# Kernel optimization log

Hardware: AMD Instinct MI355X
Metric: run time of the kernel (lower is better)

Reference implementation:

```python
import jax, jax.numpy as jnp
import numpy as np

B, M, S, N, DIN, C = 2048, 5, 128, 128, 64, 32
MID = C // 2  # 16
EPS = 1e-5
NEG_SLOPE = 0.2


def setup_inputs() -> dict:
    key = jax.random.key(0)
    ks = jax.random.split(key, 13)
    sc = lambda fan: 1.0 / np.sqrt(fan)
    return {
        "x_global": jax.random.normal(ks[0], (B, N, C), jnp.float32),
        "x_local": jax.random.normal(ks[1], (B * M, S, DIN), jnp.float32),
        "W_lin": jax.random.normal(ks[2], (C, DIN), jnp.float32) * sc(DIN),
        "b_lin": jnp.zeros((C,), jnp.float32),
        "W_att": jax.random.normal(ks[3], (C,), jnp.float32) * sc(C),  # Conv2d(C,1,1) weight
        "Wa": jax.random.normal(ks[4], (MID, C), jnp.float32) * sc(C),
        "Wb": jax.random.normal(ks[5], (MID, C), jnp.float32) * sc(C),
        "Wc": jax.random.normal(ks[6], (MID, C), jnp.float32) * sc(C),
        "Wn": jax.random.normal(ks[7], (MID, MID), jnp.float32) * sc(MID),
        "Wl": jax.random.normal(ks[8], (MID, MID), jnp.float32) * sc(MID),
        "Wd": jax.random.normal(ks[9], (C, 2 * MID), jnp.float32) * sc(2 * MID),
        "bn_gamma": jnp.ones((C,), jnp.float32),
        "bn_beta": jnp.zeros((C,), jnp.float32),
    }


def reference(x_global, x_local, W_lin, b_lin, W_att, Wa, Wb, Wc, Wn, Wl, Wd, bn_gamma, bn_beta):
    # --- Motion_Aggregation_Module.forward ---
    xl = x_local.reshape(B, M, S, DIN)
    xl = jnp.einsum('bmsd,cd->bmsc', xl, W_lin) + b_lin          # Linear(64,32)
    curves = jnp.transpose(xl, (0, 3, 1, 2))                      # [B,C,M,S]
    x = jnp.transpose(x_global, (0, 2, 1))                        # [B,C,N]

    # --- Correlation_Module.forward ---
    att = jnp.einsum('c,bcms->bms', W_att, curves)                # line_conv_att -> [B,M,S]
    inter = jnp.einsum('bcms,bms->bcm', curves, jax.nn.softmax(att, axis=-1))  # [B,C,M]
    intra = jnp.einsum('bcms,bms->bcs', curves, jax.nn.softmax(att, axis=-2))  # [B,C,S]

    inter = jnp.einsum('oc,bcm->bom', Wa, inter)                  # conva -> [B,MID,M]
    intra = jnp.einsum('oc,bcs->bos', Wb, intra)                  # convb -> [B,MID,S]
    x_logits = jnp.einsum('oc,bcn->bno', Wc, x)                   # convc^T -> [B,N,MID]

    a_inter = jax.nn.softmax(jnp.einsum('bno,bom->bnm', x_logits, inter), axis=-1)  # [B,N,M]
    a_intra = jax.nn.softmax(jnp.einsum('bno,bos->bns', x_logits, intra), axis=-1)  # [B,N,S]

    v_inter = jnp.einsum('po,bom->bmp', Wn, inter)                # convn^T -> [B,M,MID]
    v_intra = jnp.einsum('po,bos->bsp', Wl, intra)                # convl^T -> [B,S,MID]

    f_inter = jnp.einsum('bnm,bmp->bnp', a_inter, v_inter)        # [B,N,MID]
    f_intra = jnp.einsum('bns,bsp->bnp', a_intra, v_intra)        # [B,N,MID]
    feat = jnp.concatenate([f_inter, f_intra], axis=-1)           # [B,N,2*MID]
    feat = jnp.einsum('oc,bnc->bon', Wd, feat)                    # convd conv -> [B,C,N]

    # BatchNorm1d (training mode: batch stats over (B, N), biased variance)
    mean = feat.mean(axis=(0, 2), keepdims=True)
    var = feat.var(axis=(0, 2), keepdims=True)
    feat = (feat - mean) * jax.lax.rsqrt(var + EPS)
    feat = feat * bn_gamma[None, :, None] + bn_beta[None, :, None]

    out = x + feat                                                # residual
    out = jnp.where(out >= 0, out, NEG_SLOPE * out)               # leaky_relu(0.2)
    return jnp.transpose(out, (0, 2, 1))                          # [B,N,C]
```

## Files before the change

kernel.cpp:

```cpp
#include <hip/hip_runtime.h>
#include <math.h>

#define NB 2048
typedef float f32x4 __attribute__((ext_vector_type(4)));
typedef float f32x2 __attribute__((ext_vector_type(2)));

#define P_WAL 0
#define P_WBL 1024
#define P_WLBL 2048
#define P_WNAL 3072
#define P_WEFF 4096
#define P_BWA 4160
#define P_BWB 4176
#define P_BWL 4192
#define P_BWN 4208
#define P_C0  4224

#define WS_BNPART 4352
#define WS_COEF   135424
#define WS_SMALL  135488
#define WS_BIG_I  463168
#define WS_BIG_V  (463168 + 4194304)
#define WS_FEAT16 (463168 + 8388608)

__device__ __forceinline__ unsigned short f2bf(float f) {
  unsigned int u = __float_as_uint(f);
  u += 0x7fffu + ((u >> 16) & 1u);
  return (unsigned short)(u >> 16);
}
__device__ __forceinline__ unsigned int pack2bf(float lo, float hi) {
  return (unsigned int)f2bf(lo) | ((unsigned int)f2bf(hi) << 16);
}
__device__ __forceinline__ float bflo(unsigned int u) { return __uint_as_float(u << 16); }
__device__ __forceinline__ float bfhi(unsigned int u) { return __uint_as_float(u & 0xffff0000u); }

#define BSTAGE(MASK, HALF)                                        \
  { const bool hi_ = (lane & (MASK)) != 0;                        \
    _Pragma("unroll")                                             \
    for (int k_ = 0; k_ < (HALF); ++k_) {                         \
      float mine_ = hi_ ? a[k_ + (HALF)] : a[k_];                 \
      float oth_  = hi_ ? a[k_] : a[k_ + (HALF)];                 \
      a[k_] = mine_ + __shfl_xor(oth_, (MASK));                   \
    } }

__global__ __launch_bounds__(256) void k0_pre(const float* __restrict__ W_lin,
                                              const float* __restrict__ b_lin,
                                              const float* __restrict__ W_att,
                                              const float* __restrict__ Wa,
                                              const float* __restrict__ Wb,
                                              const float* __restrict__ Wn,
                                              const float* __restrict__ Wl,
                                              float* __restrict__ pre) {
  int t = threadIdx.x;
  for (int i = t; i < 1024; i += 256) {
    int o = i >> 6, d = i & 63;
    float sa = 0.f, sb = 0.f;
    for (int c = 0; c < 32; ++c) {
      float wl = W_lin[c * 64 + d];
      sa += Wa[o * 32 + c] * wl;
      sb += Wb[o * 32 + c] * wl;
    }
    pre[P_WAL + i] = sa;
    pre[P_WBL + i] = sb;
  }
  if (t < 64) {
    float s = 0.f;
    for (int c = 0; c < 32; ++c) s += W_att[c] * W_lin[c * 64 + t];
    pre[P_WEFF + t] = s;
  }
  if (t < 16) {
    float sa = 0.f, sb = 0.f;
    for (int c = 0; c < 32; ++c) {
      sa += Wa[t * 32 + c] * b_lin[c];
      sb += Wb[t * 32 + c] * b_lin[c];
    }
    pre[P_BWA + t] = sa;
    pre[P_BWB + t] = sb;
  }
  if (t == 0) {
    float s = 0.f;
    for (int c = 0; c < 32; ++c) s += W_att[c] * b_lin[c];
    pre[P_C0] = s;
  }
  __syncthreads();
  for (int i = t; i < 1024; i += 256) {
    int p_ = i >> 6, d = i & 63;
    float sl = 0.f, sn = 0.f;
    for (int o = 0; o < 16; ++o) {
      sl += Wl[p_ * 16 + o] * pre[P_WBL + o * 64 + d];
      sn += Wn[p_ * 16 + o] * pre[P_WAL + o * 64 + d];
    }
    pre[P_WLBL + i] = sl;
    pre[P_WNAL + i] = sn;
  }
  if (t < 16) {
    float sl = 0.f, sn = 0.f;
    for (int o = 0; o < 16; ++o) {
      sl += Wl[t * 16 + o] * pre[P_BWB + o];
      sn += Wn[t * 16 + o] * pre[P_BWA + o];
    }
    pre[P_BWL + t] = sl;
    pre[P_BWN + t] = sn;
  }
}

__global__ __launch_bounds__(1024, 2) void k1a(
    const float* __restrict__ xl_all, const float* __restrict__ pre,
    float* __restrict__ p_small, float* __restrict__ bigI,
    float* __restrict__ bigV) {
  __shared__ __align__(16) float xaggi[128 * 68];
  __shared__ f32x4 scratch5[5][16][16];
  __shared__ float pe[5][16];
  __shared__ float xagg_inter[5][64];

  const int t = threadIdx.x;
  const int b = blockIdx.x;
  const int lane = t & 63;
  const int w = t >> 6;
  const int q = lane >> 4;
  const int i16 = lane & 15;

  const float* xl = xl_all + (size_t)b * (5 * 128 * 64);
  const f32x4 weff4 = ((const f32x4*)(pre + P_WEFF))[i16];
  const float c0 = pre[P_C0];

  const float* xb = xl + (size_t)(8 * w + q) * 64 + 4 * i16;

  f32x4 xA[2], xB[2], acc[2];
  float Zk[2];
  #pragma unroll
  for (int k = 0; k < 2; ++k) {
    acc[k] = (f32x4)0.f;
    Zk[k] = 0.f;
    xA[k] = *(const f32x4*)(xb + k * 256);
  }

  #pragma unroll
  for (int m = 0; m < 5; ++m) {
    f32x4* xc = (m & 1) ? xB : xA;
    f32x4* xn = (m & 1) ? xA : xB;
    if (m < 4) {
      const float* np = xb + (size_t)(m + 1) * 8192;
      #pragma unroll
      for (int k = 0; k < 2; ++k) xn[k] = *(const f32x4*)(np + k * 256);
    }
    float a0, a1;
    {
      f32x4 p0 = xc[0] * weff4, p1 = xc[1] * weff4;
      a0 = p0.x + p0.y + p0.z + p0.w;
      a1 = p1.x + p1.y + p1.z + p1.w;
    }
    #pragma unroll
    for (int mask = 1; mask <= 8; mask <<= 1) {
      a0 += __shfl_xor(a0, mask);
      a1 += __shfl_xor(a1, mask);
    }
    float e0 = __expf(a0 + c0), e1 = __expf(a1 + c0);
    Zk[0] += e0; Zk[1] += e1;
    f32x4 pim;
    {
      f32x4 pr0 = e0 * xc[0];
      f32x4 pr1 = e1 * xc[1];
      acc[0] += pr0; acc[1] += pr1;
      pim = pr0 + pr1;
    }
    float se = e0 + e1;
    #pragma unroll
    for (int mask = 16; mask <= 32; mask <<= 1) {
      pim.x += __shfl_xor(pim.x, mask);
      pim.y += __shfl_xor(pim.y, mask);
      pim.z += __shfl_xor(pim.z, mask);
      pim.w += __shfl_xor(pim.w, mask);
      se += __shfl_xor(se, mask);
    }
    if (lane < 16) {
      scratch5[m][w][i16] = pim;
      if (i16 == 0) pe[m][w] = se;
    }
  }

  #pragma unroll
  for (int k = 0; k < 2; ++k) {
    float invz = 1.f / Zk[k];
    f32x4 v = acc[k] * invz;
    int r = 8 * w + 4 * k + q;
    *(f32x4*)&xaggi[r * 68 + 4 * i16] = v;
  }
  __syncthreads();

  if (t < 320) {
    int mm = t >> 6, d = t & 63;
    const float* sp = (const float*)&scratch5[mm][0][0];
    float s = 0.f;
    #pragma unroll
    for (int j = 0; j < 16; ++j) s += sp[j * 64 + d];
    float sume = 0.f;
    #pragma unroll
    for (int j = 0; j < 16; ++j) sume += pe[mm][j];
    xagg_inter[mm][d] = s / sume;
  }
  __syncthreads();

  if (t < 512) {
    const int q2 = __builtin_amdgcn_readfirstlane(t >> 7);
    const int s2 = t & 127;
    const float* Wbase = pre + ((q2 < 2) ? P_WBL : P_WLBL) + (q2 & 1) * 512;
    const float* xrow = &xaggi[s2 * 68];
    float acc2[8];
    #pragma unroll
    for (int r = 0; r < 8; ++r) acc2[r] = 0.f;
    #pragma unroll
    for (int c = 0; c < 64; c += 4) {
      f32x4 xa = *(const f32x4*)(xrow + c);
      #pragma unroll
      for (int r = 0; r < 8; ++r)
        acc2[r] += xa.x * Wbase[r * 64 + c] + xa.y * Wbase[r * 64 + c + 1] +
                   xa.z * Wbase[r * 64 + c + 2] + xa.w * Wbase[r * 64 + c + 3];
    }
    const int bb = ((q2 < 2) ? P_BWB : P_BWL) + (q2 & 1) * 8;
    float* dst = ((q2 < 2) ? bigI : bigV) + (size_t)b * 2048 + s2 * 16 + (q2 & 1) * 8;
    f32x4 o0, o1;
    o0.x = acc2[0] + pre[bb + 0];
    o0.y = acc2[1] + pre[bb + 1];
    o0.z = acc2[2] + pre[bb + 2];
    o0.w = acc2[3] + pre[bb + 3];
    o1.x = acc2[4] + pre[bb + 4];
    o1.y = acc2[5] + pre[bb + 5];
    o1.z = acc2[6] + pre[bb + 6];
    o1.w = acc2[7] + pre[bb + 7];
    *(f32x4*)dst = o0;
    *(f32x4*)(dst + 4) = o1;
  } else if (t < 672) {
    int tt = t - 512;
    int o2 = tt & 31, mm = tt >> 5;
    const float* wr = pre + ((o2 < 16) ? (P_WAL + o2 * 64) : (P_WNAL + (o2 - 16) * 64));
    float p = 0.f;
    #pragma unroll
    for (int d = 0; d < 64; ++d) p += wr[d] * xagg_inter[mm][d];
    p += (o2 < 16) ? pre[P_BWA + o2] : pre[P_BWN + (o2 - 16)];
    float* os = p_small + (size_t)b * 160;
    if (o2 < 16) os[mm * 16 + o2] = p;
    else os[80 + mm * 16 + (o2 - 16)] = p;
  }
}

__global__ __launch_bounds__(128, 1) void k1b(
    const float* __restrict__ xg_all, const float* __restrict__ Wc_g,
    const float* __restrict__ Wd_g, const float* __restrict__ p_small,
    const float* __restrict__ bigI, const float* __restrict__ bigV,
    unsigned int* __restrict__ feat16, float* __restrict__ bn_part) {
  __shared__ f32x4 slabI[128][4];
  __shared__ f32x4 slabV[128][4];
  __shared__ float part1[2][32];
  __shared__ float part2[2][32];

  const int t = threadIdx.x;
  const int b = blockIdx.x;
  const int lane = t & 63;
  const int w = t >> 6;
  const int kmap = ((lane & 1) << 4) | ((lane & 2) << 2) | (lane & 4) |
                   ((lane >> 2) & 2) | ((lane >> 4) & 1);

  const f32x4* gI = (const f32x4*)(bigI + (size_t)b * 2048);
  const f32x4* gV = (const f32x4*)(bigV + (size_t)b * 2048);
  #pragma unroll
  for (int j = 0; j < 4; ++j) {
    ((f32x4*)slabI)[t + 128 * j] = gI[t + 128 * j];
    ((f32x4*)slabV)[t + 128 * j] = gV[t + 128 * j];
  }

  const f32x4* xgr = (const f32x4*)(xg_all + ((size_t)b * 128 + t) * 32);
  f32x4 xv[8];
  #pragma unroll
  for (int j = 0; j < 8; ++j) xv[j] = xgr[j];
  f32x4 xl4[4];
  #pragma unroll
  for (int o4 = 0; o4 < 4; ++o4) {
    f32x4 r;
    #pragma unroll
    for (int jj = 0; jj < 4; ++jj) {
      const int o = o4 * 4 + jj;
      f32x4 s = (f32x4)0.f;
      #pragma unroll
      for (int j = 0; j < 8; ++j) s += xv[j] * *(const f32x4*)(Wc_g + o * 32 + 4 * j);
      r[jj] = s.x + s.y + s.z + s.w;
    }
    xl4[o4] = r;
  }
  __syncthreads();

  float sum = 0.f;
  f32x4 fa[4];
  #pragma unroll
  for (int j = 0; j < 4; ++j) fa[j] = (f32x4)0.f;
  for (int i = 0; i < 128; ++i) {
    f32x4 d4 = xl4[0] * slabI[i][0] + xl4[1] * slabI[i][1] +
               xl4[2] * slabI[i][2] + xl4[3] * slabI[i][3];
    float e = __expf(d4.x + d4.y + d4.z + d4.w);
    sum += e;
    #pragma unroll
    for (int j = 0; j < 4; ++j) fa[j] += e * slabV[i][j];
  }
  const float inv = 1.f / sum;
  f32x4 fin[4];
  #pragma unroll
  for (int j = 0; j < 4; ++j) fin[j] = fa[j] * inv;

  const float* sm = p_small + (size_t)b * 160;
  float L[5], mx3 = -1e30f;
  #pragma unroll
  for (int mm = 0; mm < 5; ++mm) {
    float p = 0.f;
    #pragma unroll
    for (int o4 = 0; o4 < 4; ++o4) {
      #pragma unroll
      for (int jj = 0; jj < 4; ++jj) p += xl4[o4][jj] * sm[mm * 16 + o4 * 4 + jj];
    }
    L[mm] = p;
    mx3 = fmaxf(mx3, p);
  }
  float sum3 = 0.f;
  #pragma unroll
  for (int mm = 0; mm < 5; ++mm) { L[mm] = __expf(L[mm] - mx3); sum3 += L[mm]; }
  const float inv3 = 1.f / sum3;
  f32x4 fi[4];
  #pragma unroll
  for (int o4 = 0; o4 < 4; ++o4) {
    f32x4 r;
    #pragma unroll
    for (int jj = 0; jj < 4; ++jj) {
      float p = 0.f;
      #pragma unroll
      for (int mm = 0; mm < 5; ++mm) p += L[mm] * sm[80 + mm * 16 + o4 * 4 + jj];
      r[jj] = p * inv3;
    }
    fi[o4] = r;
  }

  f32x4 feat[8];
  #pragma unroll
  for (int o4 = 0; o4 < 8; ++o4) {
    f32x4 r;
    #pragma unroll
    for (int jj = 0; jj < 4; ++jj) {
      const int o = o4 * 4 + jj;
      f32x4 s = (f32x4)0.f;
      #pragma unroll
      for (int j = 0; j < 4; ++j) {
        s += fi[j]  * *(const f32x4*)(Wd_g + o * 32 + 4 * j);
        s += fin[j] * *(const f32x4*)(Wd_g + o * 32 + 16 + 4 * j);
      }
      r[jj] = s.x + s.y + s.z + s.w;
    }
    feat[o4] = r;
  }
  {
    unsigned int* op = feat16 + ((size_t)b * 128 + t) * 16;
    uint4 u0, u1, u2, u3;
    u0.x = pack2bf(feat[0].x, feat[0].y); u0.y = pack2bf(feat[0].z, feat[0].w);
    u0.z = pack2bf(feat[1].x, feat[1].y); u0.w = pack2bf(feat[1].z, feat[1].w);
    u1.x = pack2bf(feat[2].x, feat[2].y); u1.y = pack2bf(feat[2].z, feat[2].w);
    u1.z = pack2bf(feat[3].x, feat[3].y); u1.w = pack2bf(feat[3].z, feat[3].w);
    u2.x = pack2bf(feat[4].x, feat[4].y); u2.y = pack2bf(feat[4].z, feat[4].w);
    u2.z = pack2bf(feat[5].x, feat[5].y); u2.w = pack2bf(feat[5].z, feat[5].w);
    u3.x = pack2bf(feat[6].x, feat[6].y); u3.y = pack2bf(feat[6].z, feat[6].w);
    u3.z = pack2bf(feat[7].x, feat[7].y); u3.w = pack2bf(feat[7].z, feat[7].w);
    ((uint4*)op)[0] = u0;
    ((uint4*)op)[1] = u1;
    ((uint4*)op)[2] = u2;
    ((uint4*)op)[3] = u3;
  }

  {
    float a[32];
    #pragma unroll
    for (int o = 0; o < 32; ++o) a[o] = feat[o >> 2][o & 3];
    BSTAGE(1, 16) BSTAGE(2, 8) BSTAGE(4, 4) BSTAGE(8, 2) BSTAGE(16, 1)
    a[0] += __shfl_xor(a[0], 32);
    if (lane < 32) part1[w][kmap] = a[0];
  }
  {
    float a[32];
    #pragma unroll
    for (int o = 0; o < 32; ++o) { float v = feat[o >> 2][o & 3]; a[o] = v * v; }
    BSTAGE(1, 16) BSTAGE(2, 8) BSTAGE(4, 4) BSTAGE(8, 2) BSTAGE(16, 1)
    a[0] += __shfl_xor(a[0], 32);
    if (lane < 32) part2[w][kmap] = a[0];
  }
  __syncthreads();
  if (t < 64) {
    int c = t & 31, h = t >> 5;
    float v = h ? (part2[0][c] + part2[1][c]) : (part1[0][c] + part1[1][c]);
    bn_part[(size_t)b * 64 + h * 32 + c] = v;
  }
}

__global__ __launch_bounds__(256, 1) void k2_stats(const float* __restrict__ bn_part,
                                                   const float* __restrict__ gamma,
                                                   const float* __restrict__ beta,
                                                   float* __restrict__ coef) {
  __shared__ float red[2][4];
  const int c = blockIdx.x;
  const int t = threadIdx.x;
  const int lane = t & 63, w = t >> 6;
  float s1 = 0.f, s2 = 0.f;
  for (int bb = t; bb < NB; bb += 256) {
    s1 += bn_part[(size_t)bb * 64 + c];
    s2 += bn_part[(size_t)bb * 64 + c + 32];
  }
  #pragma unroll
  for (int mask = 1; mask <= 32; mask <<= 1) {
    s1 += __shfl_xor(s1, mask);
    s2 += __shfl_xor(s2, mask);
  }
  if (lane == 0) { red[0][w] = s1; red[1][w] = s2; }
  __syncthreads();
  if (t == 0) {
    float S1 = red[0][0] + red[0][1] + red[0][2] + red[0][3];
    float S2 = red[1][0] + red[1][1] + red[1][2] + red[1][3];
    const float inv = 1.f / (float)(NB * 128);
    float mean = S1 * inv;
    float var = S2 * inv - mean * mean;
    float scl = gamma[c] * rsqrtf(var + 1e-5f);
    coef[c] = scl;
    coef[32 + c] = beta[c] - mean * scl;
  }
}

__global__ __launch_bounds__(256) void k3_final(const float* __restrict__ xg,
                                                const unsigned int* __restrict__ feat16,
                                                float* __restrict__ out,
                                                const float* __restrict__ coef) {
  __shared__ float s_c[64];
  if (threadIdx.x < 64) s_c[threadIdx.x] = coef[threadIdx.x];
  __syncthreads();
  size_t i4 = (size_t)blockIdx.x * 256 + threadIdx.x;
  uint2 fu = ((const uint2*)feat16)[i4];
  float4 x = ((const float4*)xg)[i4];
  int c = (int)((i4 * 4) & 31);
  float4 r;
  r.x = x.x + bflo(fu.x) * s_c[c + 0] + s_c[32 + c + 0];
  r.y = x.y + bfhi(fu.x) * s_c[c + 1] + s_c[32 + c + 1];
  r.z = x.z + bflo(fu.y) * s_c[c + 2] + s_c[32 + c + 2];
  r.w = x.w + bfhi(fu.y) * s_c[c + 3] + s_c[32 + c + 3];
  r.x = r.x >= 0.f ? r.x : 0.2f * r.x;
  r.y = r.y >= 0.f ? r.y : 0.2f * r.y;
  r.z = r.z >= 0.f ? r.z : 0.2f * r.z;
  r.w = r.w >= 0.f ? r.w : 0.2f * r.w;
  ((float4*)out)[i4] = r;
}

extern "C" void kernel_launch(void* const* d_in, const int* in_sizes, int n_in,
                              void* d_out, int out_size, void* d_ws, size_t ws_size,
                              hipStream_t stream) {
  const float* xg    = (const float*)d_in[0];
  const float* xl    = (const float*)d_in[1];
  const float* W_lin = (const float*)d_in[2];
  const float* b_lin = (const float*)d_in[3];
  const float* W_att = (const float*)d_in[4];
  const float* Wa    = (const float*)d_in[5];
  const float* Wb    = (const float*)d_in[6];
  const float* Wc    = (const float*)d_in[7];
  const float* Wn    = (const float*)d_in[8];
  const float* Wl    = (const float*)d_in[9];
  const float* Wd    = (const float*)d_in[10];
  const float* gamma = (const float*)d_in[11];
  const float* beta  = (const float*)d_in[12];
  float* out = (float*)d_out;
  float* ws = (float*)d_ws;
  float* pre = ws;
  float* bn_part = ws + WS_BNPART;
  float* coef = ws + WS_COEF;
  float* p_small = ws + WS_SMALL;
  float* bigI = ws + WS_BIG_I;
  float* bigV = ws + WS_BIG_V;
  unsigned int* feat16 = (unsigned int*)(ws + WS_FEAT16);

  hipLaunchKernelGGL(k0_pre, dim3(1), dim3(256), 0, stream,
                     W_lin, b_lin, W_att, Wa, Wb, Wn, Wl, pre);
  hipLaunchKernelGGL(k1a, dim3(NB), dim3(1024), 0, stream, xl, pre, p_small, bigI, bigV);
  hipLaunchKernelGGL(k1b, dim3(NB), dim3(128), 0, stream,
                     xg, Wc, Wd, p_small, bigI, bigV, feat16, bn_part);
  hipLaunchKernelGGL(k2_stats, dim3(32), dim3(256), 0, stream, bn_part, gamma, beta, coef);
  hipLaunchKernelGGL(k3_final, dim3(8192), dim3(256), 0, stream, xg, feat16, out, coef);
}
```

Before: 196.7 us.

## Merge k1a and k1b into one kernel keeping intermediates in shared memory

Fuses the per-batch aggregation kernel and the attention/projection kernel into a single 1024-thread kernel. The bigI/bigV/p_small intermediates stay in LDS and are no longer written to and re-read from global memory, which removes about 33 MB of traffic and one launch. The second stage is re-partitioned across 8 threads per row instead of 1, with shuffle reductions, and the Wc projection overlaps with the inter-aggregation phase. The cost is heavier LDS use per block, which may cut occupancy, plus extra shuffle work.

```diff
diff --git a/kernel.cpp b/kernel.cpp
--- a/kernel.cpp
+++ b/kernel.cpp
@@ -18,10 +18,7 @@
 
 #define WS_BNPART 4352
 #define WS_COEF   135424
-#define WS_SMALL  135488
-#define WS_BIG_I  463168
-#define WS_BIG_V  (463168 + 4194304)
-#define WS_FEAT16 (463168 + 8388608)
+#define WS_FEAT16 140000
 
 __device__ __forceinline__ unsigned short f2bf(float f) {
   unsigned int u = __float_as_uint(f);
@@ -104,14 +101,23 @@
   }
 }
 
-__global__ __launch_bounds__(1024, 2) void k1a(
-    const float* __restrict__ xl_all, const float* __restrict__ pre,
-    float* __restrict__ p_small, float* __restrict__ bigI,
-    float* __restrict__ bigV) {
+__global__ __launch_bounds__(1024, 2) void k1_merged(
+    const float* __restrict__ xl_all, const float* __restrict__ xg_all,
+    const float* __restrict__ pre, const float* __restrict__ Wc_g,
+    const float* __restrict__ Wd_g, unsigned int* __restrict__ feat16,
+    float* __restrict__ bn_part) {
   __shared__ __align__(16) float xaggi[128 * 68];
-  __shared__ f32x4 scratch5[5][16][16];
-  __shared__ float pe[5][16];
-  __shared__ float xagg_inter[5][64];
+  __shared__ __align__(16) float RU[5120];
+  __shared__ __align__(16) float xlogL[128 * 20];
+  __shared__ float s_Wd[32][33];
+  __shared__ float pe[80];
+  __shared__ float xagg_inter[320];
+  __shared__ float s_small[160];
+  __shared__ float part1[16][33];
+  __shared__ float part2[16][33];
+
+  float* slabI = RU;
+  float* slabV = RU + 2560;
 
   const int t = threadIdx.x;
   const int b = blockIdx.x;
@@ -119,13 +125,16 @@
   const int w = t >> 6;
   const int q = lane >> 4;
   const int i16 = lane & 15;
+  const int n2 = t >> 3;
+  const int q3 = t & 7;
 
   const float* xl = xl_all + (size_t)b * (5 * 128 * 64);
   const f32x4 weff4 = ((const f32x4*)(pre + P_WEFF))[i16];
   const float c0 = pre[P_C0];
 
+  if (t < 1024) { int i = t; if (i < 1024) s_Wd[i >> 5][i & 31] = Wd_g[i]; }
+
   const float* xb = xl + (size_t)(8 * w + q) * 64 + 4 * i16;
-
   f32x4 xA[2], xB[2], acc[2];
   float Zk[2];
   #pragma unroll
@@ -134,7 +143,6 @@
     Zk[k] = 0.f;
     xA[k] = *(const f32x4*)(xb + k * 256);
   }
-
   #pragma unroll
   for (int m = 0; m < 5; ++m) {
     f32x4* xc = (m & 1) ? xB : xA;
@@ -174,11 +182,10 @@
       se += __shfl_xor(se, mask);
     }
     if (lane < 16) {
-      scratch5[m][w][i16] = pim;
-      if (i16 == 0) pe[m][w] = se;
-    }
-  }
-
+      ((f32x4*)RU)[(m * 16 + w) * 16 + i16] = pim;
+      if (i16 == 0) pe[m * 16 + w] = se;
+    }
+  }
   #pragma unroll
   for (int k = 0; k < 2; ++k) {
     float invz = 1.f / Zk[k];
@@ -190,14 +197,27 @@
 
   if (t < 320) {
     int mm = t >> 6, d = t & 63;
-    const float* sp = (const float*)&scratch5[mm][0][0];
+    const float* sp = RU + mm * 1024;
     float s = 0.f;
     #pragma unroll
     for (int j = 0; j < 16; ++j) s += sp[j * 64 + d];
     float sume = 0.f;
     #pragma unroll
-    for (int j = 0; j < 16; ++j) sume += pe[mm][j];
-    xagg_inter[mm][d] = s / sume;
+    for (int j = 0; j < 16; ++j) sume += pe[mm * 16 + j];
+    xagg_inter[mm * 64 + d] = s / sume;
+  } else if (t >= 896) {
+    int n = t - 896;
+    const f32x4* xgr = (const f32x4*)(xg_all + ((size_t)b * 128 + n) * 32);
+    f32x4 xv[8];
+    #pragma unroll
+    for (int j = 0; j < 8; ++j) xv[j] = xgr[j];
+    #pragma unroll
+    for (int o = 0; o < 16; ++o) {
+      f32x4 s = (f32x4)0.f;
+      #pragma unroll
+      for (int j = 0; j < 8; ++j) s += xv[j] * *(const f32x4*)(Wc_g + o * 32 + 4 * j);
+      xlogL[n * 20 + o] = s.x + s.y + s.z + s.w;
+    }
   }
   __syncthreads();
 
@@ -218,7 +238,7 @@
                    xa.z * Wbase[r * 64 + c + 2] + xa.w * Wbase[r * 64 + c + 3];
     }
     const int bb = ((q2 < 2) ? P_BWB : P_BWL) + (q2 & 1) * 8;
-    float* dst = ((q2 < 2) ? bigI : bigV) + (size_t)b * 2048 + s2 * 16 + (q2 & 1) * 8;
+    float* dst = ((q2 < 2) ? slabI : slabV) + s2 * 20 + (q2 & 1) * 8;
     f32x4 o0, o1;
     o0.x = acc2[0] + pre[bb + 0];
     o0.y = acc2[1] + pre[bb + 1];
@@ -236,85 +256,55 @@
     const float* wr = pre + ((o2 < 16) ? (P_WAL + o2 * 64) : (P_WNAL + (o2 - 16) * 64));
     float p = 0.f;
     #pragma unroll
-    for (int d = 0; d < 64; ++d) p += wr[d] * xagg_inter[mm][d];
+    for (int d = 0; d < 64; ++d) p += wr[d] * xagg_inter[mm * 64 + d];
     p += (o2 < 16) ? pre[P_BWA + o2] : pre[P_BWN + (o2 - 16)];
-    float* os = p_small + (size_t)b * 160;
-    if (o2 < 16) os[mm * 16 + o2] = p;
-    else os[80 + mm * 16 + (o2 - 16)] = p;
-  }
-}
-
-__global__ __launch_bounds__(128, 1) void k1b(
-    const float* __restrict__ xg_all, const float* __restrict__ Wc_g,
-    const float* __restrict__ Wd_g, const float* __restrict__ p_small,
-    const float* __restrict__ bigI, const float* __restrict__ bigV,
-    unsigned int* __restrict__ feat16, float* __restrict__ bn_part) {
-  __shared__ f32x4 slabI[128][4];
-  __shared__ f32x4 slabV[128][4];
-  __shared__ float part1[2][32];
-  __shared__ float part2[2][32];
-
-  const int t = threadIdx.x;
-  const int b = blockIdx.x;
-  const int lane = t & 63;
-  const int w = t >> 6;
-  const int kmap = ((lane & 1) << 4) | ((lane & 2) << 2) | (lane & 4) |
-                   ((lane >> 2) & 2) | ((lane >> 4) & 1);
-
-  const f32x4* gI = (const f32x4*)(bigI + (size_t)b * 2048);
-  const f32x4* gV = (const f32x4*)(bigV + (size_t)b * 2048);
-  #pragma unroll
-  for (int j = 0; j < 4; ++j) {
-    ((f32x4*)slabI)[t + 128 * j] = gI[t + 128 * j];
-    ((f32x4*)slabV)[t + 128 * j] = gV[t + 128 * j];
-  }
-
-  const f32x4* xgr = (const f32x4*)(xg_all + ((size_t)b * 128 + t) * 32);
-  f32x4 xv[8];
-  #pragma unroll
-  for (int j = 0; j < 8; ++j) xv[j] = xgr[j];
-  f32x4 xl4[4];
-  #pragma unroll
-  for (int o4 = 0; o4 < 4; ++o4) {
-    f32x4 r;
-    #pragma unroll
-    for (int jj = 0; jj < 4; ++jj) {
-      const int o = o4 * 4 + jj;
-      f32x4 s = (f32x4)0.f;
-      #pragma unroll
-      for (int j = 0; j < 8; ++j) s += xv[j] * *(const f32x4*)(Wc_g + o * 32 + 4 * j);
-      r[jj] = s.x + s.y + s.z + s.w;
-    }
-    xl4[o4] = r;
-  }
-  __syncthreads();
-
+    if (o2 < 16) s_small[mm * 16 + o2] = p;
+    else s_small[80 + mm * 16 + (o2 - 16)] = p;
+  }
+  __syncthreads();
+
+  f32x4 xlg[4];
+  #pragma unroll
+  for (int c = 0; c < 4; ++c) xlg[c] = *(const f32x4*)&xlogL[n2 * 20 + 4 * c];
   float sum = 0.f;
-  f32x4 fa[4];
-  #pragma unroll
-  for (int j = 0; j < 4; ++j) fa[j] = (f32x4)0.f;
-  for (int i = 0; i < 128; ++i) {
-    f32x4 d4 = xl4[0] * slabI[i][0] + xl4[1] * slabI[i][1] +
-               xl4[2] * slabI[i][2] + xl4[3] * slabI[i][3];
+  f32x4 fav[4];
+  #pragma unroll
+  for (int c = 0; c < 4; ++c) fav[c] = (f32x4)0.f;
+  #pragma unroll 4
+  for (int k = 0; k < 16; ++k) {
+    const int i = q3 + 8 * k;
+    const f32x4* rI = (const f32x4*)&slabI[i * 20];
+    f32x4 d4 = xlg[0] * rI[0] + xlg[1] * rI[1] + xlg[2] * rI[2] + xlg[3] * rI[3];
     float e = __expf(d4.x + d4.y + d4.z + d4.w);
     sum += e;
-    #pragma unroll
-    for (int j = 0; j < 4; ++j) fa[j] += e * slabV[i][j];
+    const f32x4* rV = (const f32x4*)&slabV[i * 20];
+    #pragma unroll
+    for (int c = 0; c < 4; ++c) fav[c] += e * rV[c];
+  }
+  #pragma unroll
+  for (int mask = 1; mask <= 4; mask <<= 1) {
+    sum += __shfl_xor(sum, mask);
+    #pragma unroll
+    for (int c = 0; c < 4; ++c) {
+      fav[c].x += __shfl_xor(fav[c].x, mask);
+      fav[c].y += __shfl_xor(fav[c].y, mask);
+      fav[c].z += __shfl_xor(fav[c].z, mask);
+      fav[c].w += __shfl_xor(fav[c].w, mask);
+    }
   }
   const float inv = 1.f / sum;
   f32x4 fin[4];
   #pragma unroll
-  for (int j = 0; j < 4; ++j) fin[j] = fa[j] * inv;
-
-  const float* sm = p_small + (size_t)b * 160;
+  for (int c = 0; c < 4; ++c) fin[c] = fav[c] * inv;
+
   float L[5], mx3 = -1e30f;
   #pragma unroll
   for (int mm = 0; mm < 5; ++mm) {
     float p = 0.f;
     #pragma unroll
-    for (int o4 = 0; o4 < 4; ++o4) {
-      #pragma unroll
-      for (int jj = 0; jj < 4; ++jj) p += xl4[o4][jj] * sm[mm * 16 + o4 * 4 + jj];
+    for (int c = 0; c < 4; ++c) {
+      #pragma unroll
+      for (int jj = 0; jj < 4; ++jj) p += xlg[c][jj] * s_small[mm * 16 + 4 * c + jj];
     }
     L[mm] = p;
     mx3 = fmaxf(mx3, p);
@@ -325,72 +315,61 @@
   const float inv3 = 1.f / sum3;
   f32x4 fi[4];
   #pragma unroll
-  for (int o4 = 0; o4 < 4; ++o4) {
+  for (int c = 0; c < 4; ++c) {
     f32x4 r;
     #pragma unroll
     for (int jj = 0; jj < 4; ++jj) {
       float p = 0.f;
       #pragma unroll
-      for (int mm = 0; mm < 5; ++mm) p += L[mm] * sm[80 + mm * 16 + o4 * 4 + jj];
+      for (int mm = 0; mm < 5; ++mm) p += L[mm] * s_small[80 + mm * 16 + 4 * c + jj];
       r[jj] = p * inv3;
     }
-    fi[o4] = r;
-  }
-
-  f32x4 feat[8];
-  #pragma unroll
-  for (int o4 = 0; o4 < 8; ++o4) {
-    f32x4 r;
-    #pragma unroll
-    for (int jj = 0; jj < 4; ++jj) {
-      const int o = o4 * 4 + jj;
-      f32x4 s = (f32x4)0.f;
-      #pragma unroll
-      for (int j = 0; j < 4; ++j) {
-        s += fi[j]  * *(const f32x4*)(Wd_g + o * 32 + 4 * j);
-        s += fin[j] * *(const f32x4*)(Wd_g + o * 32 + 16 + 4 * j);
+    fi[c] = r;
+  }
+  float fo[4];
+  #pragma unroll
+  for (int j = 0; j < 4; ++j) {
+    const int o = 4 * q3 + j;
+    float p = 0.f;
+    #pragma unroll
+    for (int c = 0; c < 4; ++c) {
+      #pragma unroll
+      for (int jj = 0; jj < 4; ++jj) {
+        p += fi[c][jj] * s_Wd[o][4 * c + jj];
+        p += fin[c][jj] * s_Wd[o][16 + 4 * c + jj];
       }
-      r[jj] = s.x + s.y + s.z + s.w;
-    }
-    feat[o4] = r;
+    }
+    fo[j] = p;
   }
   {
-    unsigned int* op = feat16 + ((size_t)b * 128 + t) * 16;
-    uint4 u0, u1, u2, u3;
-    u0.x = pack2bf(feat[0].x, feat[0].y); u0.y = pack2bf(feat[0].z, feat[0].w);
-    u0.z = pack2bf(feat[1].x, feat[1].y); u0.w = pack2bf(feat[1].z, feat[1].w);
-    u1.x = pack2bf(feat[2].x, feat[2].y); u1.y = pack2bf(feat[2].z, feat[2].w);
-    u1.z = pack2bf(feat[3].x, feat[3].y); u1.w = pack2bf(feat[3].z, feat[3].w);
-    u2.x = pack2bf(feat[4].x, feat[4].y); u2.y = pack2bf(feat[4].z, feat[4].w);
-    u2.z = pack2bf(feat[5].x, feat[5].y); u2.w = pack2bf(feat[5].z, feat[5].w);
-    u3.x = pack2bf(feat[6].x, feat[6].y); u3.y = pack2bf(feat[6].z, feat[6].w);
-    u3.z = pack2bf(feat[7].x, feat[7].y); u3.w = pack2bf(feat[7].z, feat[7].w);
-    ((uint4*)op)[0] = u0;
-    ((uint4*)op)[1] = u1;
-    ((uint4*)op)[2] = u2;
-    ((uint4*)op)[3] = u3;
-  }
-
+    uint2 u;
+    u.x = pack2bf(fo[0], fo[1]);
+    u.y = pack2bf(fo[2], fo[3]);
+    ((uint2*)feat16)[(size_t)b * 1024 + n2 * 8 + q3] = u;
+  }
+  const int omap = 4 * q3 + 2 * ((lane >> 3) & 1) + ((lane >> 4) & 1);
   {
-    float a[32];
-    #pragma unroll
-    for (int o = 0; o < 32; ++o) a[o] = feat[o >> 2][o & 3];
-    BSTAGE(1, 16) BSTAGE(2, 8) BSTAGE(4, 4) BSTAGE(8, 2) BSTAGE(16, 1)
+    float a[4];
+    #pragma unroll
+    for (int j = 0; j < 4; ++j) a[j] = fo[j];
+    BSTAGE(8, 2) BSTAGE(16, 1)
     a[0] += __shfl_xor(a[0], 32);
-    if (lane < 32) part1[w][kmap] = a[0];
+    if (lane < 32) part1[w][omap] = a[0];
   }
   {
-    float a[32];
-    #pragma unroll
-    for (int o = 0; o < 32; ++o) { float v = feat[o >> 2][o & 3]; a[o] = v * v; }
-    BSTAGE(1, 16) BSTAGE(2, 8) BSTAGE(4, 4) BSTAGE(8, 2) BSTAGE(16, 1)
+    float a[4];
+    #pragma unroll
+    for (int j = 0; j < 4; ++j) a[j] = fo[j] * fo[j];
+    BSTAGE(8, 2) BSTAGE(16, 1)
     a[0] += __shfl_xor(a[0], 32);
-    if (lane < 32) part2[w][kmap] = a[0];
+    if (lane < 32) part2[w][omap] = a[0];
   }
   __syncthreads();
   if (t < 64) {
     int c = t & 31, h = t >> 5;
-    float v = h ? (part2[0][c] + part2[1][c]) : (part1[0][c] + part1[1][c]);
+    float v = 0.f;
+    #pragma unroll
+    for (int j = 0; j < 16; ++j) v += h ? part2[j][c] : part1[j][c];
     bn_part[(size_t)b * 64 + h * 32 + c] = v;
   }
 }
@@ -471,16 +450,12 @@
   float* pre = ws;
   float* bn_part = ws + WS_BNPART;
   float* coef = ws + WS_COEF;
-  float* p_small = ws + WS_SMALL;
-  float* bigI = ws + WS_BIG_I;
-  float* bigV = ws + WS_BIG_V;
   unsigned int* feat16 = (unsigned int*)(ws + WS_FEAT16);
 
   hipLaunchKernelGGL(k0_pre, dim3(1), dim3(256), 0, stream,
                      W_lin, b_lin, W_att, Wa, Wb, Wn, Wl, pre);
-  hipLaunchKernelGGL(k1a, dim3(NB), dim3(1024), 0, stream, xl, pre, p_small, bigI, bigV);
-  hipLaunchKernelGGL(k1b, dim3(NB), dim3(128), 0, stream,
-                     xg, Wc, Wd, p_small, bigI, bigV, feat16, bn_part);
+  hipLaunchKernelGGL(k1_merged, dim3(NB), dim3(1024), 0, stream,
+                     xl, xg, pre, Wc, Wd, feat16, bn_part);
   hipLaunchKernelGGL(k2_stats, dim3(32), dim3(256), 0, stream, bn_part, gamma, beta, coef);
   hipLaunchKernelGGL(k3_final, dim3(8192), dim3(256), 0, stream, xg, feat16, out, coef);
 }
```

Measured after the change: 246.1 us. 25.1% more time.

## Split k1b softmax-attention loop across four waves with LDS reduction

Applied to the files above, without the earlier changes.

k1b now launches 256 threads per batch instead of 128. Each wave handles a quarter of the 128 intra keys for two query rows, and the partial exp-sums and weighted value accumulators are reduced through padded shared memory. The xlogit projection and p_small values are staged in LDS, and the slabs are padded to a row stride of 20 to avoid bank conflicts. This is meant to shorten the serial 128-iteration loop per thread and raise occupancy, at the cost of extra barriers, a shared-memory reduction and more LDS use.

```diff
diff --git a/kernel.cpp b/kernel.cpp
--- a/kernel.cpp
+++ b/kernel.cpp
@@ -244,13 +244,16 @@
   }
 }
 
-__global__ __launch_bounds__(128, 1) void k1b(
+__global__ __launch_bounds__(256, 4) void k1b(
     const float* __restrict__ xg_all, const float* __restrict__ Wc_g,
     const float* __restrict__ Wd_g, const float* __restrict__ p_small,
     const float* __restrict__ bigI, const float* __restrict__ bigV,
     unsigned int* __restrict__ feat16, float* __restrict__ bn_part) {
-  __shared__ f32x4 slabI[128][4];
-  __shared__ f32x4 slabV[128][4];
+  __shared__ __align__(16) float UN[10240];
+  float* slabI = UN;
+  float* slabV = UN + 2560;
+  float* xlogL = UN + 5120;
+  __shared__ float s_sm[160];
   __shared__ float part1[2][32];
   __shared__ float part2[2][32];
 
@@ -258,134 +261,216 @@
   const int b = blockIdx.x;
   const int lane = t & 63;
   const int w = t >> 6;
-  const int kmap = ((lane & 1) << 4) | ((lane & 2) << 2) | (lane & 4) |
-                   ((lane >> 2) & 2) | ((lane >> 4) & 1);
-
-  const f32x4* gI = (const f32x4*)(bigI + (size_t)b * 2048);
-  const f32x4* gV = (const f32x4*)(bigV + (size_t)b * 2048);
+
+  {
+    const f32x4* gI = (const f32x4*)(bigI + (size_t)b * 2048);
+    const f32x4* gV = (const f32x4*)(bigV + (size_t)b * 2048);
+    #pragma unroll
+    for (int j = 0; j < 2; ++j) {
+      int idx = t + 256 * j;
+      int row = idx >> 2, c4 = idx & 3;
+      *(f32x4*)&slabI[row * 20 + 4 * c4] = gI[idx];
+      *(f32x4*)&slabV[row * 20 + 4 * c4] = gV[idx];
+    }
+  }
+  if (t < 128) {
+    const int n = t;
+    const f32x4* xgr = (const f32x4*)(xg_all + ((size_t)b * 128 + n) * 32);
+    f32x4 xv[8];
+    #pragma unroll
+    for (int j = 0; j < 8; ++j) xv[j] = xgr[j];
+    #pragma unroll
+    for (int o4 = 0; o4 < 4; ++o4) {
+      f32x4 r;
+      #pragma unroll
+      for (int jj = 0; jj < 4; ++jj) {
+        const int o = o4 * 4 + jj;
+        f32x4 s = (f32x4)0.f;
+        #pragma unroll
+        for (int j = 0; j < 8; ++j) s += xv[j] * *(const f32x4*)(Wc_g + o * 32 + 4 * j);
+        r[jj] = s.x + s.y + s.z + s.w;
+      }
+      *(f32x4*)&xlogL[n * 20 + 4 * o4] = r;
+    }
+  }
+  if (t >= 96) {
+    int i2 = t - 96;
+    s_sm[i2] = p_small[(size_t)b * 160 + i2];
+  }
+  __syncthreads();
+
+  const int n0 = lane, n1 = lane + 64;
+  f32x4 xlg0[4], xlg1[4];
   #pragma unroll
-  for (int j = 0; j < 4; ++j) {
-    ((f32x4*)slabI)[t + 128 * j] = gI[t + 128 * j];
-    ((f32x4*)slabV)[t + 128 * j] = gV[t + 128 * j];
-  }
-
-  const f32x4* xgr = (const f32x4*)(xg_all + ((size_t)b * 128 + t) * 32);
-  f32x4 xv[8];
+  for (int c = 0; c < 4; ++c) {
+    xlg0[c] = *(const f32x4*)&xlogL[n0 * 20 + 4 * c];
+    xlg1[c] = *(const f32x4*)&xlogL[n1 * 20 + 4 * c];
+  }
+
+  float s0 = 0.f, s1 = 0.f;
+  f32x4 fav0[4], fav1[4];
   #pragma unroll
-  for (int j = 0; j < 8; ++j) xv[j] = xgr[j];
-  f32x4 xl4[4];
-  #pragma unroll
-  for (int o4 = 0; o4 < 4; ++o4) {
-    f32x4 r;
-    #pragma unroll
-    for (int jj = 0; jj < 4; ++jj) {
-      const int o = o4 * 4 + jj;
-      f32x4 s = (f32x4)0.f;
-      #pragma unroll
-      for (int j = 0; j < 8; ++j) s += xv[j] * *(const f32x4*)(Wc_g + o * 32 + 4 * j);
-      r[jj] = s.x + s.y + s.z + s.w;
-    }
-    xl4[o4] = r;
-  }
-  __syncthreads();
-
-  float sum = 0.f;
-  f32x4 fa[4];
-  #pragma unroll
-  for (int j = 0; j < 4; ++j) fa[j] = (f32x4)0.f;
-  for (int i = 0; i < 128; ++i) {
-    f32x4 d4 = xl4[0] * slabI[i][0] + xl4[1] * slabI[i][1] +
-               xl4[2] * slabI[i][2] + xl4[3] * slabI[i][3];
-    float e = __expf(d4.x + d4.y + d4.z + d4.w);
-    sum += e;
-    #pragma unroll
-    for (int j = 0; j < 4; ++j) fa[j] += e * slabV[i][j];
-  }
-  const float inv = 1.f / sum;
-  f32x4 fin[4];
-  #pragma unroll
-  for (int j = 0; j < 4; ++j) fin[j] = fa[j] * inv;
-
-  const float* sm = p_small + (size_t)b * 160;
-  float L[5], mx3 = -1e30f;
-  #pragma unroll
-  for (int mm = 0; mm < 5; ++mm) {
-    float p = 0.f;
+  for (int c = 0; c < 4; ++c) { fav0[c] = (f32x4)0.f; fav1[c] = (f32x4)0.f; }
+  for (int k = 0; k < 32; ++k) {
+    const int i = 32 * w + k;
+    const f32x4* rI = (const f32x4*)&slabI[i * 20];
+    f32x4 d0 = xlg0[0] * rI[0] + xlg0[1] * rI[1] + xlg0[2] * rI[2] + xlg0[3] * rI[3];
+    f32x4 d1 = xlg1[0] * rI[0] + xlg1[1] * rI[1] + xlg1[2] * rI[2] + xlg1[3] * rI[3];
+    float e0 = __expf(d0.x + d0.y + d0.z + d0.w);
+    float e1 = __expf(d1.x + d1.y + d1.z + d1.w);
+    s0 += e0; s1 += e1;
+    const f32x4* rV = (const f32x4*)&slabV[i * 20];
+    #pragma unroll
+    for (int c = 0; c < 4; ++c) {
+      f32x4 v = rV[c];
+      fav0[c] += e0 * v;
+      fav1[c] += e1 * v;
+    }
+  }
+  __syncthreads();
+
+  {
+    float* c0p = UN + w * 2560 + n0 * 20;
+    float* c1p = UN + w * 2560 + n1 * 20;
+    #pragma unroll
+    for (int c = 0; c < 4; ++c) {
+      *(f32x4*)&c0p[4 * c] = fav0[c];
+      *(f32x4*)&c1p[4 * c] = fav1[c];
+    }
+    c0p[16] = s0;
+    c1p[16] = s1;
+  }
+  __syncthreads();
+
+  {
+    const int n = t & 127, g = t >> 7;
+    if (g == 0) {
+      f32x4 a0 = (f32x4)0.f, a1 = (f32x4)0.f;
+      #pragma unroll
+      for (int ww = 0; ww < 4; ++ww) {
+        const float* cp = UN + ww * 2560 + n * 20;
+        a0 += *(const f32x4*)&cp[0];
+        a1 += *(const f32x4*)&cp[4];
+      }
+      float* dp = UN + n * 20;
+      *(f32x4*)&dp[0] = a0;
+      *(f32x4*)&dp[4] = a1;
+    } else {
+      f32x4 a2 = (f32x4)0.f, a3 = (f32x4)0.f;
+      float as = 0.f;
+      #pragma unroll
+      for (int ww = 0; ww < 4; ++ww) {
+        const float* cp = UN + ww * 2560 + n * 20;
+        a2 += *(const f32x4*)&cp[8];
+        a3 += *(const f32x4*)&cp[12];
+        as += cp[16];
+      }
+      float* dp = UN + n * 20;
+      *(f32x4*)&dp[8] = a2;
+      *(f32x4*)&dp[12] = a3;
+      dp[16] = as;
+    }
+  }
+  __syncthreads();
+
+  if (t < 128) {
+    const int n = t;
+    const float* cp = UN + n * 20;
+    f32x4 fav[4];
+    #pragma unroll
+    for (int c = 0; c < 4; ++c) fav[c] = *(const f32x4*)&cp[4 * c];
+    const float inv = 1.f / cp[16];
+    f32x4 fin[4];
+    #pragma unroll
+    for (int c = 0; c < 4; ++c) fin[c] = fav[c] * inv;
+
+    f32x4 xme[4];
+    #pragma unroll
+    for (int c = 0; c < 4; ++c) xme[c] = (t < 64) ? xlg0[c] : xlg1[c];
+
+    float L[5], mx3 = -1e30f;
+    #pragma unroll
+    for (int mm = 0; mm < 5; ++mm) {
+      float p = 0.f;
+      #pragma unroll
+      for (int c = 0; c < 4; ++c) {
+        #pragma unroll
+        for (int jj = 0; jj < 4; ++jj) p += xme[c][jj] * s_sm[mm * 16 + 4 * c + jj];
+      }
+      L[mm] = p;
+      mx3 = fmaxf(mx3, p);
+    }
+    float sum3 = 0.f;
+    #pragma unroll
+    for (int mm = 0; mm < 5; ++mm) { L[mm] = __expf(L[mm] - mx3); sum3 += L[mm]; }
+    const float inv3 = 1.f / sum3;
+    f32x4 fi[4];
     #pragma unroll
     for (int o4 = 0; o4 < 4; ++o4) {
-      #pragma unroll
-      for (int jj = 0; jj < 4; ++jj) p += xl4[o4][jj] * sm[mm * 16 + o4 * 4 + jj];
-    }
-    L[mm] = p;
-    mx3 = fmaxf(mx3, p);
-  }
-  float sum3 = 0.f;
-  #pragma unroll
-  for (int mm = 0; mm < 5; ++mm) { L[mm] = __expf(L[mm] - mx3); sum3 += L[mm]; }
-  const float inv3 = 1.f / sum3;
-  f32x4 fi[4];
-  #pragma unroll
-  for (int o4 = 0; o4 < 4; ++o4) {
-    f32x4 r;
-    #pragma unroll
-    for (int jj = 0; jj < 4; ++jj) {
-      float p = 0.f;
-      #pragma unroll
-      for (int mm = 0; mm < 5; ++mm) p += L[mm] * sm[80 + mm * 16 + o4 * 4 + jj];
-      r[jj] = p * inv3;
-    }
-    fi[o4] = r;
-  }
-
-  f32x4 feat[8];
-  #pragma unroll
-  for (int o4 = 0; o4 < 8; ++o4) {
-    f32x4 r;
-    #pragma unroll
-    for (int jj = 0; jj < 4; ++jj) {
-      const int o = o4 * 4 + jj;
-      f32x4 s = (f32x4)0.f;
-      #pragma unroll
-      for (int j = 0; j < 4; ++j) {
-        s += fi[j]  * *(const f32x4*)(Wd_g + o * 32 + 4 * j);
-        s += fin[j] * *(const f32x4*)(Wd_g + o * 32 + 16 + 4 * j);
+      f32x4 r;
+      #pragma unroll
+      for (int jj = 0; jj < 4; ++jj) {
+        float p = 0.f;
+        #pragma unroll
+        for (int mm = 0; mm < 5; ++mm) p += L[mm] * s_sm[80 + mm * 16 + o4 * 4 + jj];
+        r[jj] = p * inv3;
       }
-      r[jj] = s.x + s.y + s.z + s.w;
-    }
-    feat[o4] = r;
-  }
-  {
-    unsigned int* op = feat16 + ((size_t)b * 128 + t) * 16;
-    uint4 u0, u1, u2, u3;
-    u0.x = pack2bf(feat[0].x, feat[0].y); u0.y = pack2bf(feat[0].z, feat[0].w);
-    u0.z = pack2bf(feat[1].x, feat[1].y); u0.w = pack2bf(feat[1].z, feat[1].w);
-    u1.x = pack2bf(feat[2].x, feat[2].y); u1.y = pack2bf(feat[2].z, feat[2].w);
-    u1.z = pack2bf(feat[3].x, feat[3].y); u1.w = pack2bf(feat[3].z, feat[3].w);
-    u2.x = pack2bf(feat[4].x, feat[4].y); u2.y = pack2bf(feat[4].z, feat[4].w);
-    u2.z = pack2bf(feat[5].x, feat[5].y); u2.w = pack2bf(feat[5].z, feat[5].w);
-    u3.x = pack2bf(feat[6].x, feat[6].y); u3.y = pack2bf(feat[6].z, feat[6].w);
-    u3.z = pack2bf(feat[7].x, feat[7].y); u3.w = pack2bf(feat[7].z, feat[7].w);
-    ((uint4*)op)[0] = u0;
-    ((uint4*)op)[1] = u1;
-    ((uint4*)op)[2] = u2;
-    ((uint4*)op)[3] = u3;
-  }
-
-  {
-    float a[32];
-    #pragma unroll
-    for (int o = 0; o < 32; ++o) a[o] = feat[o >> 2][o & 3];
-    BSTAGE(1, 16) BSTAGE(2, 8) BSTAGE(4, 4) BSTAGE(8, 2) BSTAGE(16, 1)
-    a[0] += __shfl_xor(a[0], 32);
-    if (lane < 32) part1[w][kmap] = a[0];
-  }
-  {
-    float a[32];
-    #pragma unroll
-    for (int o = 0; o < 32; ++o) { float v = feat[o >> 2][o & 3]; a[o] = v * v; }
-    BSTAGE(1, 16) BSTAGE(2, 8) BSTAGE(4, 4) BSTAGE(8, 2) BSTAGE(16, 1)
-    a[0] += __shfl_xor(a[0], 32);
-    if (lane < 32) part2[w][kmap] = a[0];
+      fi[o4] = r;
+    }
+
+    f32x4 feat[8];
+    #pragma unroll
+    for (int o4 = 0; o4 < 8; ++o4) {
+      f32x4 r;
+      #pragma unroll
+      for (int jj = 0; jj < 4; ++jj) {
+        const int o = o4 * 4 + jj;
+        f32x4 s = (f32x4)0.f;
+        #pragma unroll
+        for (int j = 0; j < 4; ++j) {
+          s += fi[j]  * *(const f32x4*)(Wd_g + o * 32 + 4 * j);
+          s += fin[j] * *(const f32x4*)(Wd_g + o * 32 + 16 + 4 * j);
+        }
+        r[jj] = s.x + s.y + s.z + s.w;
+      }
+      feat[o4] = r;
+    }
+    {
+      unsigned int* op = feat16 + ((size_t)b * 128 + n) * 16;
+      uint4 u0, u1, u2, u3;
+      u0.x = pack2bf(feat[0].x, feat[0].y); u0.y = pack2bf(feat[0].z, feat[0].w);
+      u0.z = pack2bf(feat[1].x, feat[1].y); u0.w = pack2bf(feat[1].z, feat[1].w);
+      u1.x = pack2bf(feat[2].x, feat[2].y); u1.y = pack2bf(feat[2].z, feat[2].w);
+      u1.z = pack2bf(feat[3].x, feat[3].y); u1.w = pack2bf(feat[3].z, feat[3].w);
+      u2.x = pack2bf(feat[4].x, feat[4].y); u2.y = pack2bf(feat[4].z, feat[4].w);
+      u2.z = pack2bf(feat[5].x, feat[5].y); u2.w = pack2bf(feat[5].z, feat[5].w);
+      u3.x = pack2bf(feat[6].x, feat[6].y); u3.y = pack2bf(feat[6].z, feat[6].w);
+      u3.z = pack2bf(feat[7].x, feat[7].y); u3.w = pack2bf(feat[7].z, feat[7].w);
+      ((uint4*)op)[0] = u0;
+      ((uint4*)op)[1] = u1;
+      ((uint4*)op)[2] = u2;
+      ((uint4*)op)[3] = u3;
+    }
+
+    const int w2 = t >> 6;
+    const int kmap = ((lane & 1) << 4) | ((lane & 2) << 2) | (lane & 4) |
+                     ((lane >> 2) & 2) | ((lane >> 4) & 1);
+    {
+      float a[32];
+      #pragma unroll
+      for (int o = 0; o < 32; ++o) a[o] = feat[o >> 2][o & 3];
+      BSTAGE(1, 16) BSTAGE(2, 8) BSTAGE(4, 4) BSTAGE(8, 2) BSTAGE(16, 1)
+      a[0] += __shfl_xor(a[0], 32);
+      if (lane < 32) part1[w2][kmap] = a[0];
+    }
+    {
+      float a[32];
+      #pragma unroll
+      for (int o = 0; o < 32; ++o) { float v = feat[o >> 2][o & 3]; a[o] = v * v; }
+      BSTAGE(1, 16) BSTAGE(2, 8) BSTAGE(4, 4) BSTAGE(8, 2) BSTAGE(16, 1)
+      a[0] += __shfl_xor(a[0], 32);
+      if (lane < 32) part2[w2][kmap] = a[0];
+    }
   }
   __syncthreads();
   if (t < 64) {
@@ -479,7 +564,7 @@
   hipLaunchKernelGGL(k0_pre, dim3(1), dim3(256), 0, stream,
                      W_lin, b_lin, W_att, Wa, Wb, Wn, Wl, pre);
   hipLaunchKernelGGL(k1a, dim3(NB), dim3(1024), 0, stream, xl, pre, p_small, bigI, bigV);
-  hipLaunchKernelGGL(k1b, dim3(NB), dim3(128), 0, stream,
+  hipLaunchKernelGGL(k1b, dim3(NB), dim3(256), 0, stream,
                      xg, Wc, Wd, p_small, bigI, bigV, feat16, bn_part);
   hipLaunchKernelGGL(k2_stats, dim3(32), dim3(256), 0, stream, bn_part, gamma, beta, coef);
   hipLaunchKernelGGL(k3_final, dim3(8192), dim3(256), 0, stream, xg, feat16, out, coef);
```

New measurement: 195.9 us. No clear change (-0.4%).
